# Optimization experiments

Hardware: AMD Instinct MI355X
Metric: run time of the kernel (lower is better)

Reference implementation:

```python
import jax, jax.numpy as jnp
import numpy as np
import math

TAU = 2.0
V_TH = 1.0
DECAY = math.exp(-1.0 / TAU)  # LIF membrane decay


def setup_inputs() -> dict:
    key = jax.random.key(0)
    k_x, k_w, k_b = jax.random.split(key, 3)
    T, B, C_IN, H, W = 4, 8, 64, 128, 128
    C_OUT, K = 64, 3
    x = jax.random.normal(k_x, (T, B, C_IN, H, W), dtype=jnp.float32)
    fan_in = C_IN * K * K
    weight = jax.random.normal(k_w, (C_OUT, C_IN, K, K), dtype=jnp.float32) / jnp.sqrt(fan_in)
    bias = jax.random.normal(k_b, (C_OUT,), dtype=jnp.float32) * 0.01
    return {"x": x, "weight": weight, "bias": bias}


def reference(x, weight, bias):
    # x: [T, B, C_IN, H, W]; 3x3 conv, stride 1, pad 1 -> same spatial size
    T, B, C_IN, H, W = x.shape
    C_OUT = weight.shape[0]

    def conv(x_t):
        y = jax.lax.conv_general_dilated(
            x_t, weight,
            window_strides=(1, 1),
            padding=((1, 1), (1, 1)),
            dimension_numbers=("NCHW", "OIHW", "NCHW"),
        )
        return y + bias[None, :, None, None]

    def step(v, x_t):
        v_temp = v * DECAY + conv(x_t)            # membrane decay + synaptic input
        spike = (v_temp > V_TH).astype(v_temp.dtype)  # threshold fire
        v_next = v_temp * (1.0 - spike)           # soft reset
        return v_next, spike

    v0 = jnp.zeros((B, C_OUT, H, W), dtype=jnp.float32)
    _, spikes = jax.lax.scan(step, v0, x)         # spikes: [T, B, C_OUT, H, W]
    return spikes
```

## Files before the change

### kernel.cpp

```cpp
#include <hip/hip_runtime.h>

#define T_STEPS 4
#define BATCH   8
#define C_IN    64
#define C_OUT   64
#define HH      128
#define WW      128
#define TH      8
#define TW      16
#define ROWS    (TH + 2)
#define COLS    18
#define CPAD    68

#define DECAY_F32 0.6065306597126334f

__global__ void wt_build_kernel(const float* __restrict__ w, float* __restrict__ wt) {
    int tid = blockIdx.x * blockDim.x + threadIdx.x;
    if (tid >= 9 * C_IN * C_OUT) return;
    int co = tid & 63;
    int ci = (tid >> 6) & 63;
    int j  = tid >> 12;
    wt[tid] = w[(co * C_IN + ci) * 9 + j];
}

__global__ __launch_bounds__(512) void snn_exact_kernel(
    const float* __restrict__ x,
    const float* __restrict__ wt,
    const float* __restrict__ bias,
    float* __restrict__ out)
{
    __shared__ __align__(16) float sx[ROWS * COLS * CPAD];

    const int tid  = threadIdx.x;
    const int wid  = __builtin_amdgcn_readfirstlane(tid >> 6);
    const int lane = tid & 63;
    const int y    = lane & 3;
    const int xcol = lane >> 2;
    const int sy   = (wid >> 2) << 2;
    const int cob  = (wid & 3) << 4;
    const int b    = blockIdx.z;
    const int gy0  = blockIdx.y * TH;
    const int gx0  = blockIdx.x * TW;

    const float* bp = bias + cob;

    const float* xbase = &sx[((sy + y) * COLS + xcol) * CPAD];

    float v[16];
#pragma unroll
    for (int o = 0; o < 16; ++o) v[o] = 0.0f;

    for (int t = 0; t < T_STEPS; ++t) {
        __syncthreads();
        const float* xsrc = x + ((size_t)(t * BATCH + b) * C_IN) * (HH * WW);
        for (int e = tid; e < C_IN * ROWS * COLS; e += 512) {
            int ci  = e / (ROWS * COLS);
            int rem = e - ci * (ROWS * COLS);
            int row = rem / COLS;
            int col = rem - row * COLS;
            int gy  = gy0 + row - 1;
            int gx  = gx0 + col - 1;
            float val = 0.0f;
            if ((unsigned)gy < (unsigned)HH && (unsigned)gx < (unsigned)WW)
                val = xsrc[ci * (HH * WW) + gy * WW + gx];
            sx[(row * COLS + col) * CPAD + ci] = val;
        }
        __syncthreads();

        float acc[16];
#pragma unroll
        for (int o = 0; o < 16; ++o) acc[o] = 0.0f;

#define TAP(KY, KX)                                                                   \
        {                                                                             \
            const float* wj = wt + ((KY) * 3 + (KX)) * (C_IN * C_OUT) + cob;          \
            const float* xt = xbase + ((KY) * COLS + (KX)) * CPAD;                    \
            _Pragma("unroll 2")                                                       \
            for (int ci0 = 0; ci0 < C_IN; ci0 += 4) {                                 \
                const float4 xv = *reinterpret_cast<const float4*>(xt + ci0);         \
                const float xq[4] = {xv.x, xv.y, xv.z, xv.w};                         \
                _Pragma("unroll")                                                     \
                for (int k = 0; k < 4; ++k) {                                         \
                    const float* wp = wj + ((ci0 + k) << 6);                          \
                    _Pragma("unroll")                                                 \
                    for (int o = 0; o < 16; ++o)                                      \
                        acc[o] = fmaf(xq[k], wp[o], acc[o]);                          \
                }                                                                     \
            }                                                                         \
        }

        TAP(0, 0) TAP(0, 1) TAP(0, 2)
        TAP(1, 0) TAP(1, 1) TAP(1, 2)
        TAP(2, 0) TAP(2, 1) TAP(2, 2)
#undef TAP

        float* obase = out + ((size_t)(t * BATCH + b) * C_OUT + cob) * (HH * WW)
                     + (gy0 + sy + y) * WW + gx0 + xcol;
#pragma unroll
        for (int o = 0; o < 16; ++o) {
            float cb = __fadd_rn(acc[o], bp[o]);
            float vt = __fadd_rn(__fmul_rn(v[o], DECAY_F32), cb);
            bool fire = vt > 1.0f;
            v[o] = fire ? 0.0f : vt;
            obase[(size_t)o * (HH * WW)] = fire ? 1.0f : 0.0f;
        }
    }
}

extern "C" void kernel_launch(void* const* d_in, const int* in_sizes, int n_in,
                              void* d_out, int out_size, void* d_ws, size_t ws_size,
                              hipStream_t stream) {
    const float* x    = (const float*)d_in[0];
    const float* w    = (const float*)d_in[1];
    const float* bias = (const float*)d_in[2];
    float* out = (float*)d_out;
    float* wt  = (float*)d_ws;

    hipLaunchKernelGGL(wt_build_kernel, dim3((9 * C_IN * C_OUT + 255) / 256), dim3(256), 0, stream, w, wt);
    hipLaunchKernelGGL(snn_exact_kernel, dim3(WW / TW, HH / TH, BATCH), dim3(512), 0, stream,
                       x, wt, bias, out);
}
```

Measured before the change: 529.9 us.

## Shrink spatial tile to 8x8 with 256 threads and vectorize LDS halo stores

Tiles shrink from 8x16 to 8x8 pixels, blocks drop from 512 to 256 threads, and each wave now covers a full 8x8 tile for 16 output channels. The halo load writes four input channels per thread as one float4 into shared memory. Launch bounds ask for 5 blocks per CU, trading a larger halo overhead (10x10 vs 8x16 interior) for smaller LDS use per block, more blocks and higher occupancy. Output stores now cover 8 contiguous columns per row instead of 16, which may reduce write coalescing.

Measured after the change: 512.1 us. 3.4% less time.

```diff
diff --git a/kernel.cpp b/kernel.cpp
--- a/kernel.cpp
+++ b/kernel.cpp
@@ -7,9 +7,10 @@
 #define HH      128
 #define WW      128
 #define TH      8
-#define TW      16
+#define TW      8
 #define ROWS    (TH + 2)
-#define COLS    18
+#define COLS    (TW + 2)
+#define NPOS    (ROWS * COLS)
 #define CPAD    68
 
 #define DECAY_F32 0.6065306597126334f
@@ -23,28 +24,25 @@
     wt[tid] = w[(co * C_IN + ci) * 9 + j];
 }
 
-__global__ __launch_bounds__(512) void snn_exact_kernel(
+__global__ __launch_bounds__(256, 5) void snn_exact_kernel(
     const float* __restrict__ x,
     const float* __restrict__ wt,
     const float* __restrict__ bias,
     float* __restrict__ out)
 {
-    __shared__ __align__(16) float sx[ROWS * COLS * CPAD];
+    __shared__ __align__(16) float sx[NPOS * CPAD];
 
     const int tid  = threadIdx.x;
     const int wid  = __builtin_amdgcn_readfirstlane(tid >> 6);
     const int lane = tid & 63;
-    const int y    = lane & 3;
-    const int xcol = lane >> 2;
-    const int sy   = (wid >> 2) << 2;
-    const int cob  = (wid & 3) << 4;
+    const int xq_  = lane & 7;
+    const int yq_  = lane >> 3;
+    const int cob  = wid << 4;
     const int b    = blockIdx.z;
     const int gy0  = blockIdx.y * TH;
     const int gx0  = blockIdx.x * TW;
 
     const float* bp = bias + cob;
-
-    const float* xbase = &sx[((sy + y) * COLS + xcol) * CPAD];
 
     float v[16];
 #pragma unroll
@@ -53,17 +51,22 @@
     for (int t = 0; t < T_STEPS; ++t) {
         __syncthreads();
         const float* xsrc = x + ((size_t)(t * BATCH + b) * C_IN) * (HH * WW);
-        for (int e = tid; e < C_IN * ROWS * COLS; e += 512) {
-            int ci  = e / (ROWS * COLS);
-            int rem = e - ci * (ROWS * COLS);
-            int row = rem / COLS;
-            int col = rem - row * COLS;
+        for (int e = tid; e < NPOS * (C_IN / 4); e += 256) {
+            int cig = e / NPOS;
+            int pos = e - cig * NPOS;
+            int row = pos / COLS;
+            int col = pos - row * COLS;
             int gy  = gy0 + row - 1;
             int gx  = gx0 + col - 1;
-            float val = 0.0f;
-            if ((unsigned)gy < (unsigned)HH && (unsigned)gx < (unsigned)WW)
-                val = xsrc[ci * (HH * WW) + gy * WW + gx];
-            sx[(row * COLS + col) * CPAD + ci] = val;
+            float4 val = {0.f, 0.f, 0.f, 0.f};
+            if ((unsigned)gy < (unsigned)HH && (unsigned)gx < (unsigned)WW) {
+                const float* g = xsrc + (size_t)(cig << 2) * (HH * WW) + gy * WW + gx;
+                val.x = g[0];
+                val.y = g[HH * WW];
+                val.z = g[2 * HH * WW];
+                val.w = g[3 * HH * WW];
+            }
+            *reinterpret_cast<float4*>(&sx[pos * CPAD + (cig << 2)]) = val;
         }
         __syncthreads();
 
@@ -74,7 +77,7 @@
 #define TAP(KY, KX)                                                                   \
         {                                                                             \
             const float* wj = wt + ((KY) * 3 + (KX)) * (C_IN * C_OUT) + cob;          \
-            const float* xt = xbase + ((KY) * COLS + (KX)) * CPAD;                    \
+            const float* xt = &sx[((yq_ + (KY)) * COLS + (xq_ + (KX))) * CPAD];       \
             _Pragma("unroll 2")                                                       \
             for (int ci0 = 0; ci0 < C_IN; ci0 += 4) {                                 \
                 const float4 xv = *reinterpret_cast<const float4*>(xt + ci0);         \
@@ -95,7 +98,7 @@
 #undef TAP
 
         float* obase = out + ((size_t)(t * BATCH + b) * C_OUT + cob) * (HH * WW)
-                     + (gy0 + sy + y) * WW + gx0 + xcol;
+                     + (gy0 + yq_) * WW + gx0 + xq_;
 #pragma unroll
         for (int o = 0; o < 16; ++o) {
             float cb = __fadd_rn(acc[o], bp[o]);
@@ -117,6 +120,6 @@
     float* wt  = (float*)d_ws;
 
     hipLaunchKernelGGL(wt_build_kernel, dim3((9 * C_IN * C_OUT + 255) / 256), dim3(256), 0, stream, w, wt);
-    hipLaunchKernelGGL(snn_exact_kernel, dim3(WW / TW, HH / TH, BATCH), dim3(512), 0, stream,
+    hipLaunchKernelGGL(snn_exact_kernel, dim3(WW / TW, HH / TH, BATCH), dim3(256), 0, stream,
                        x, wt, bias, out);
 }
```
